# Kernel optimization log

Hardware: AMD Instinct MI355X
Metric: run time of the kernel (lower is better)

Reference implementation:

```python
import jax, jax.numpy as jnp
import numpy as np
from jax import lax

# Static config (matches init_kwargs)
DIM = 256; DR = 4; GROUP = 2; NH = 4; KS = 3; NA = 1; NUM_CLASS = 80; MUL = 5.0
CR = DIM // DR            # reduced dim = 64
GC = CR // GROUP          # offset-group channels = 32
HC = CR // NH             # per-head dim = 16
SCALE = HC ** -0.5
B, H, W = 8, 64, 64


def setup_inputs() -> dict:
    key = jax.random.key(0)
    ks_ = jax.random.split(key, 8)
    x = jax.random.normal(ks_[0], (B, DIM, H, W), jnp.float32)
    # offset = absolute pixel coordinates of the base sampling grid
    offset = jax.random.uniform(ks_[1], (B, NA * 2 * KS * KS, H, W), jnp.float32) * (H - 1)
    return dict(
        x=x, offset=offset,
        ln1_g=jnp.ones((DIM,), jnp.float32), ln1_b=jnp.zeros((DIM,), jnp.float32),
        w_qkv=jax.random.normal(ks_[2], (3 * CR, DIM), jnp.float32) * 0.02,
        w_dw=jax.random.normal(ks_[3], (GC, 1, 3, 3), jnp.float32) * 0.1,
        ln2_g=jnp.ones((GC,), jnp.float32), ln2_b=jnp.zeros((GC,), jnp.float32),
        w_off=jax.random.normal(ks_[4], (NA * 2 * KS * KS, GC, 3, 3), jnp.float32) * 0.02,
        b_off=jnp.zeros((NA * 2 * KS * KS,), jnp.float32),
        rpb_table=jax.random.normal(ks_[5], (1, NH, 1, 1, KS * KS, HC), jnp.float32) * 0.02,
        w_proj=jax.random.normal(ks_[6], (DIM, CR), jnp.float32) * 0.02,
        b_proj=jnp.zeros((DIM,), jnp.float32),
        w_cls=jax.random.normal(ks_[7], (NUM_CLASS, DIM), jnp.float32) * 0.02,
        b_cls=jnp.zeros((NUM_CLASS,), jnp.float32),
    )


def _ln_chw(x, g, b, eps=1e-5):
    # LayerNorm over channel dim of NCHW tensor (LayerNormProxy)
    xt = jnp.moveaxis(x, 1, -1)
    m = xt.mean(-1, keepdims=True)
    v = ((xt - m) ** 2).mean(-1, keepdims=True)
    y = (xt - m) * lax.rsqrt(v + eps) * g + b
    return jnp.moveaxis(y, -1, 1)


def _conv(x, w, groups=1, pad=1):
    return lax.conv_general_dilated(x, w, (1, 1), [(pad, pad), (pad, pad)],
                                    feature_group_count=groups,
                                    dimension_numbers=('NCHW', 'OIHW', 'NCHW'))


def _grid_sample(img, grid):
    # img [N,C,H,W]; grid [N,Ho,Wo,2] with (x,y) in [-1,1]; bilinear, zeros pad, align_corners=True
    N, C, Hi, Wi = img.shape
    gx = (grid[..., 0] + 1.0) * 0.5 * (Wi - 1)
    gy = (grid[..., 1] + 1.0) * 0.5 * (Hi - 1)
    x0 = jnp.floor(gx); y0 = jnp.floor(gy)
    x1 = x0 + 1.0;      y1 = y0 + 1.0

    def gather(ix, iy):
        valid = (ix >= 0) & (ix <= Wi - 1) & (iy >= 0) & (iy <= Hi - 1)
        ixc = jnp.clip(ix, 0, Wi - 1).astype(jnp.int32)
        iyc = jnp.clip(iy, 0, Hi - 1).astype(jnp.int32)
        v = jax.vmap(lambda im, yy, xx: im[:, yy, xx])(img, iyc, ixc)  # [N,C,Ho,Wo]
        return v * valid[:, None].astype(img.dtype)

    wa = ((x1 - gx) * (y1 - gy))[:, None]
    wb = ((gx - x0) * (y1 - gy))[:, None]
    wc = ((x1 - gx) * (gy - y0))[:, None]
    wd = ((gx - x0) * (gy - y0))[:, None]
    return (gather(x0, y0) * wa + gather(x1, y0) * wb +
            gather(x0, y1) * wc + gather(x1, y1) * wd)


def _extract_feats(feat, off, Hh, Ww):
    # feat [Bg,GC,H,W]; off [Bg, NA*2*KS*KS, H, W] in pixel coords (row, col)
    Bg = feat.shape[0]
    o = off.reshape(Bg, NA, KS, KS, 2, Hh, Ww)
    o = o.transpose(0, 1, 2, 5, 3, 6, 4)                  # b na kh h kw w d
    o = o.reshape(Bg, NA * KS * Hh, KS * Ww, 2)
    gy = 2.0 * o[..., 0] / (Hh - 1) - 1.0                  # row coord
    gx = 2.0 * o[..., 1] / (Ww - 1) - 1.0                  # col coord
    grid = jnp.stack([gx, gy], -1)                         # flip(-1): (x, y)
    out = _grid_sample(feat, grid)                         # [Bg,GC,NA*KS*H,KS*W]
    out = out.reshape(Bg, GC, NA, KS, Hh, KS, Ww)
    out = out.transpose(0, 2, 3, 5, 1, 4, 6).reshape(Bg, NA * KS * KS, GC, Hh, Ww)
    return out


def reference(x, offset, ln1_g, ln1_b, w_qkv, w_dw, ln2_g, ln2_b, w_off, b_off,
              rpb_table, w_proj, b_proj, w_cls, b_cls):
    Bb, C, Hh, Ww = x.shape
    N = KS * KS

    x_ = _ln_chw(x, ln1_g, ln1_b)
    qkv = jnp.einsum('oc,bchw->bohw', w_qkv, x_)           # [B,3*CR,H,W]
    q, k, v = jnp.split(qkv, 3, axis=1)                    # each [B,CR,H,W]

    # --- offset prediction ---
    q_off = q.reshape(Bb * GROUP, GC, Hh, Ww)
    t = _conv(q_off, w_dw, groups=GC)                      # depthwise 3x3
    t = _ln_chw(t, ln2_g, ln2_b)
    t = jax.nn.gelu(t, approximate=False)
    pred_offset = _conv(t, w_off) + b_off[None, :, None, None]

    off = jnp.broadcast_to(offset[:, None], (Bb, GROUP, NA * 2 * N, Hh, Ww))
    off = off.reshape(Bb * GROUP, NA * 2 * N, Hh, Ww)
    off = jnp.tanh(pred_offset) * MUL + off

    # --- deformable gather of k/v ---
    k = _extract_feats(k.reshape(Bb * GROUP, GC, Hh, Ww), off, Hh, Ww)
    v = _extract_feats(v.reshape(Bb * GROUP, GC, Hh, Ww), off, Hh, Ww)

    def to_heads(t):
        # [(b g), na*n, gc, h, w] -> [b, nh, hw, na, n, hc]
        t = t.reshape(Bb, GROUP, NA, N, GC, Hh, Ww)
        t = t.transpose(0, 5, 6, 2, 3, 1, 4)               # b h w na n g gc
        t = t.reshape(Bb, Hh * Ww, NA, N, NH, HC)
        return t.transpose(0, 4, 1, 2, 3, 5)

    k = to_heads(k) + rpb_table                            # [B,NH,HW,NA,N,HC]
    v = to_heads(v)

    q = q.reshape(Bb, NH, HC, Hh * Ww).transpose(0, 1, 3, 2)  # [B,NH,HW,HC]
    q = jnp.broadcast_to((q * SCALE)[:, :, :, None, :], (Bb, NH, Hh * Ww, NA, HC))

    attn = jnp.einsum('bnpac,bnpakc->bnpak', q, k)         # [B,NH,HW,NA,N]
    attn = jax.nn.softmax(attn, axis=-1)
    out = jnp.einsum('bnpak,bnpakc->bnpac', attn, v)       # [B,NH,HW,NA,HC]

    out = out.transpose(0, 2, 3, 1, 4).reshape(Bb, Hh * Ww, NA, CR)
    out = out @ w_proj.T + b_proj                          # [B,HW,NA,C]
    out = out + x.transpose(0, 2, 3, 1).reshape(Bb, Hh * Ww, 1, C)

    cls = out @ w_cls.T + b_cls                            # [B,HW,NA,NUM_CLASS]
    cls = cls.reshape(Bb, Hh, Ww, NA, NUM_CLASS).transpose(0, 3, 4, 1, 2)
    return cls.reshape(Bb, NA * NUM_CLASS, Hh, Ww)
```

## Files before the change

kernel.cpp:

```cpp
#include <hip/hip_runtime.h>
#include <hip/hip_fp16.h>
#include <math.h>

#define BB   8
#define HW   4096
#define BHW  32768
#define DIM  256
#define CR   64
#define GC   32
#define NHD  4
#define HC   16
#define NTAP 9
#define NCLS 80

#define OFF_QP   0u
#define OFF_QT   2097152u
#define OFF_KT   4194304u
#define OFF_T    8388608u
#define OFF_WBF  8388608u
#define OFF_AB   8437760u
#define OFF_OFFB 10485760u
#define OFF_AOT  11665408u
#define OFF_WPT  13762560u
#define OFF_WCT  13778944u
#define OFF_WFT  13799424u

typedef short bf16x8 __attribute__((ext_vector_type(8)));
typedef float f32x4  __attribute__((ext_vector_type(4)));

__device__ __forceinline__ unsigned short f2bf(float f) {
    unsigned u = __float_as_uint(f);
    unsigned r = u + 0x7FFFu + ((u >> 16) & 1u);
    return (unsigned short)(r >> 16);
}

__global__ __launch_bounds__(256) void k0_prep(
    const float* __restrict__ wqkv, const float* __restrict__ g1,
    const float* __restrict__ b1, const float* __restrict__ woff,
    const float* __restrict__ wproj, const float* __restrict__ wcls,
    float* __restrict__ ws)
{
    const int t = threadIdx.x;
    const int blk = blockIdx.x;
    if (blk < 192) {
        const int o = blk;
        unsigned short* wbf = (unsigned short*)(ws + OFF_WBF);
        wbf[o * 256 + t] = f2bf(wqkv[o * 256 + t] * g1[t]);
    } else if (blk < 448) {
        const int r = blk - 192;
        unsigned short* wpb = (unsigned short*)(ws + OFF_WPT);
        unsigned short* wcb = (unsigned short*)(ws + OFF_WCT);
        if (t < 64) wpb[r * 64 + t] = f2bf(wproj[r * 64 + t]);
        if (r < 80) wcb[r * 256 + t] = f2bf(wcls[r * 256 + t]);
    } else if (blk < 640) {
        const int o = blk - 448;
        __shared__ float sa[4], sb[4];
        float w = wqkv[o * 256 + t];
        float a = w * g1[t];
        float bb = w * b1[t];
        #pragma unroll
        for (int off = 1; off < 64; off <<= 1) {
            a  += __shfl_xor(a,  off, 64);
            bb += __shfl_xor(bb, off, 64);
        }
        const int wv = t >> 6;
        if ((t & 63) == 0) { sa[wv] = a; sb[wv] = bb; }
        __syncthreads();
        if (t == 0) {
            ws[OFF_AB + o]       = sa[0] + sa[1] + sa[2] + sa[3];
            ws[OFF_AB + 192 + o] = sb[0] + sb[1] + sb[2] + sb[3];
        }
    } else {
        int idx = (blk - 640) * 256 + t;
        if (idx < 5184) {
            int o = idx % 18;
            int rest = idx / 18;
            int ic = rest & 31, wo = rest >> 5;
            ws[OFF_WFT + idx] = woff[(o * 32 + ic) * 9 + wo];
        }
    }
}

__global__ __launch_bounds__(512) void k1_mfma(
    const float* __restrict__ x, float* __restrict__ ws)
{
    __shared__ float tile[64 * 193];
    const int t = threadIdx.x;
    const int b = blockIdx.x & 7, row = blockIdx.x >> 3;
    const int wv = __builtin_amdgcn_readfirstlane(t >> 6);
    const int pt = wv & 3, oh = wv >> 2;
    const int lane = t & 63;
    const int quad = lane >> 4, pxl = lane & 15;
    const int colbase = row * 64 + pt * 16 + pxl;
    const unsigned short* wbf = (const unsigned short*)(ws + OFF_WBF);
    const float* AB = ws + OFF_AB;

    f32x4 acc[6];
    #pragma unroll
    for (int ot = 0; ot < 6; ++ot) acc[ot] = (f32x4){0.f, 0.f, 0.f, 0.f};
    float s = 0.f, ss = 0.f;
    const size_t xb0 = (size_t)b * DIM * HW + colbase;

    for (int ks = 0; ks < 8; ++ks) {
        const int cbase = ks * 32 + quad * 8;
        float xv[8];
        #pragma unroll
        for (int j = 0; j < 8; ++j) {
            xv[j] = x[xb0 + (size_t)(cbase + j) * HW];
            s += xv[j]; ss += xv[j] * xv[j];
        }
        union { bf16x8 v; unsigned short u[8]; } bfrag;
        #pragma unroll
        for (int j = 0; j < 8; ++j) bfrag.u[j] = f2bf(xv[j]);
        #pragma unroll
        for (int ot = 0; ot < 6; ++ot) {
            const int orow = (oh * 6 + ot) * 16 + pxl;
            union { float4 f; bf16x8 v; } afrag;
            afrag.f = *(const float4*)&wbf[orow * 256 + cbase];
            acc[ot] = __builtin_amdgcn_mfma_f32_16x16x32_bf16(afrag.v, bfrag.v, acc[ot], 0, 0, 0);
        }
    }

    s  += __shfl_xor(s, 16, 64);  s  += __shfl_xor(s, 32, 64);
    ss += __shfl_xor(ss, 16, 64); ss += __shfl_xor(ss, 32, 64);
    const float m = s * (1.f / 256.f);
    const float rsv = rsqrtf(ss * (1.f / 256.f) - m * m + 1e-5f);

    const int px = pt * 16 + pxl;
    #pragma unroll
    for (int ot = 0; ot < 6; ++ot) {
        #pragma unroll
        for (int r = 0; r < 4; ++r) {
            int o = (oh * 6 + ot) * 16 + quad * 4 + r;
            tile[px * 193 + o] = rsv * (acc[ot][r] - m * AB[o]) + AB[192 + o];
        }
    }
    __syncthreads();

    float*  qp  = ws + OFF_QP;
    __half* qth = (__half*)(ws + OFF_QT);
    __half* kvh = (__half*)(ws + OFF_KT);
    const int colrow = row * 64;
    #pragma unroll
    for (int it = 0; it < 8; ++it) {
        int idx = it * 512 + t;
        int o = idx >> 6, px2 = idx & 63;
        qp[(size_t)(b * 64 + o) * HW + colrow + px2] = tile[px2 * 193 + o];
    }
    #pragma unroll
    for (int it = 0; it < 8; ++it) {
        int idx = it * 512 + t;
        int px2 = idx >> 6, o = idx & 63;
        qth[(size_t)(b * HW + colrow + px2) * 64 + o] = __float2half(tile[px2 * 193 + o]);
    }
    #pragma unroll
    for (int it = 0; it < 4; ++it) {
        int idx = it * 512 + t;
        int px2 = idx >> 5, ch32 = idx & 31;
        int sB = ch32 >> 4, ch = ch32 & 15;
        kvh[(size_t)((2 * b) * HW + colrow + px2) * 64 + sB * 32 + ch]
            = __float2half(tile[px2 * 193 + 64 + ch32]);
    }
    #pragma unroll
    for (int it = 0; it < 4; ++it) {
        int idx = it * 512 + t;
        int px2 = idx >> 5, ch32 = idx & 31;
        int sB = ch32 >> 4, ch = ch32 & 15;
        kvh[(size_t)((2 * b + 1) * HW + colrow + px2) * 64 + sB * 32 + ch]
            = __float2half(tile[px2 * 193 + 96 + ch32]);
    }
    #pragma unroll
    for (int it = 0; it < 4; ++it) {
        int idx = it * 512 + t;
        int px2 = idx >> 5, ch32 = idx & 31;
        int sB = ch32 >> 4, ch = ch32 & 15;
        kvh[(size_t)((2 * b) * HW + colrow + px2) * 64 + sB * 32 + 16 + ch]
            = __float2half(tile[px2 * 193 + 128 + ch32]);
    }
    #pragma unroll
    for (int it = 0; it < 4; ++it) {
        int idx = it * 512 + t;
        int px2 = idx >> 5, ch32 = idx & 31;
        int sB = ch32 >> 4, ch = ch32 & 15;
        kvh[(size_t)((2 * b + 1) * HW + colrow + px2) * 64 + sB * 32 + 16 + ch]
            = __float2half(tile[px2 * 193 + 160 + ch32]);
    }
}

__global__ __launch_bounds__(256) void k2_off_feat(
    const float* __restrict__ wdw, const float* __restrict__ g2, const float* __restrict__ b2,
    float* __restrict__ ws)
{
    __shared__ float qtile[3][32][64];
    __shared__ float rsum[4][64], rsq[4][64], smv[64], srv[64];
    const int t = threadIdx.x;
    const int b = blockIdx.x & 7;
    const int rest = blockIdx.x >> 3;
    const int g = rest & 1;
    const int row = rest >> 1;
    const int bg = b * 2 + g;
    const int p = t & 63;
    const int cq = __builtin_amdgcn_readfirstlane(t >> 6);
    const float* qp = ws + OFF_QP;

    #pragma unroll
    for (int it = 0; it < 6; ++it) {
        int idx = it * 256 + t;
        int rc = idx >> 4;
        int seg = (idx & 15) << 2;
        int dyy = rc >> 5, ch = rc & 31;
        int y = row + dyy - 1;
        float4 v = make_float4(0.f, 0.f, 0.f, 0.f);
        if ((unsigned)y < 64u)
            v = *(const float4*)&qp[(size_t)(b * 64 + g * 32 + ch) * HW + y * 64 + seg];
        *(float4*)&qtile[dyy][ch][seg] = v;
    }
    __syncthreads();

    float vals[8];
    float s = 0.f, ss = 0.f;
    #pragma unroll
    for (int i = 0; i < 8; ++i) {
        int ch = cq * 8 + i;
        float a = 0.f;
        #pragma unroll
        for (int dy = 0; dy < 3; ++dy) {
            #pragma unroll
            for (int dx = 0; dx < 3; ++dx) {
                int xx = p + dx - 1;
                bool vld = (unsigned)xx < 64u;
                float q = qtile[dy][ch][vld ? xx : 0];
                a += (vld ? q : 0.f) * wdw[ch * 9 + dy * 3 + dx];
            }
        }
        vals[i] = a; s += a; ss += a * a;
    }
    rsum[cq][p] = s; rsq[cq][p] = ss;
    __syncthreads();
    if (t < 64) {
        float S = rsum[0][t] + rsum[1][t] + rsum[2][t] + rsum[3][t];
        float Q = rsq[0][t] + rsq[1][t] + rsq[2][t] + rsq[3][t];
        float m = S * (1.f / 32.f);
        float v = Q * (1.f / 32.f) - m * m;
        smv[t] = m; srv[t] = rsqrtf(v + 1e-5f);
    }
    __syncthreads();
    float m = smv[p], rv = srv[p];
    float* tb = ws + OFF_T;
    #pragma unroll
    for (int i = 0; i < 8; ++i) {
        int ch = cq * 8 + i;
        float u = (vals[i] - m) * rv * g2[ch] + b2[ch];
        float ge = 0.5f * u * (1.f + erff(u * 0.70710678118654752f));
        tb[(size_t)(bg * 32 + ch) * HW + row * 64 + p] = ge;
    }
}

__global__ __launch_bounds__(256) void k3_pred_off(
    const float* __restrict__ boff, const float* __restrict__ off_in,
    float* __restrict__ ws)
{
    __shared__ float part[4 * 18 * 64];
    const int t = threadIdx.x;
    const int b = blockIdx.x & 7;
    const int rest = blockIdx.x >> 3;
    const int g = rest & 1;
    const int row = rest >> 1;
    const int bg = b * 2 + g;
    const int p = t & 63;
    const int icq = __builtin_amdgcn_readfirstlane(t >> 6);
    const float* tb = ws + OFF_T;
    const float* wfT = ws + OFF_WFT;
    float acc[18];
    #pragma unroll
    for (int o = 0; o < 18; ++o) acc[o] = 0.f;
    #pragma unroll
    for (int dy = 0; dy < 3; ++dy) {
        int y = row + dy - 1;
        if ((unsigned)y >= 64u) continue;
        #pragma unroll
        for (int dx = 0; dx < 3; ++dx) {
            int xx = p + dx - 1;
            bool vld = (unsigned)xx < 64u;
            int xc = vld ? xx : 0;
            int wo = dy * 3 + dx;
            #pragma unroll
            for (int i = 0; i < 8; ++i) {
                int ic = icq * 8 + i;
                float tv = tb[(size_t)(bg * 32 + ic) * HW + y * 64 + xc];
                tv = vld ? tv : 0.f;
                const float* wrow = wfT + (wo * 32 + ic) * 18;
                #pragma unroll
                for (int o = 0; o < 18; ++o)
                    acc[o] += tv * wrow[o];
            }
        }
    }
    #pragma unroll
    for (int o = 0; o < 18; ++o) part[(icq * 18 + o) * 64 + p] = acc[o];
    __syncthreads();
    float* ob = ws + OFF_OFFB;
    #pragma unroll
    for (int r = 0; r < 5; ++r) {
        int idx = t + r * 256;
        if (idx < 1152) {
            int o = idx >> 6, p2 = idx & 63;
            float v = part[o * 64 + p2] + part[(18 + o) * 64 + p2]
                    + part[(36 + o) * 64 + p2] + part[(54 + o) * 64 + p2] + boff[o];
            v = tanhf(v) * 5.0f + off_in[(size_t)(b * 18 + o) * HW + row * 64 + p2];
            ob[(size_t)(bg * 18 + o) * HW + row * 64 + p2] = v;
        }
    }
}

__global__ __launch_bounds__(256, 4) void k4_attn(
    const float* __restrict__ rpb, float* __restrict__ ws)
{
    __shared__ float rpb_l[NHD * NTAP * HC];
    for (int i = threadIdx.x; i < NHD * NTAP * HC; i += 256) rpb_l[i] = rpb[i];
    __syncthreads();

    const int t = threadIdx.x;
    const int wave = __builtin_amdgcn_readfirstlane(t >> 6);
    const int g = wave & 1, pxh = wave >> 1;
    const int lane = t & 63;
    const int pxl = lane & 7;
    const int prt = lane >> 3;
    const int s    = prt >> 2;
    const int half = (prt >> 1) & 1;
    const int j    = prt & 1;
    const int b = blockIdx.x & 7;
    const int chunk = blockIdx.x >> 3;
    const int hw = chunk * 16 + pxh * 8 + pxl;
    const int pix = b * HW + hw;
    const int bg = b * 2 + g;
    const int head = g * 2 + s;

    const __half* qth = (const __half*)(ws + OFF_QT);
    const __half* kvh = (const __half*)(ws + OFF_KT);
    const float*  ob  = ws + OFF_OFFB;

    float rr_[NTAP], cc_[NTAP];
    #pragma unroll
    for (int n = 0; n < NTAP; ++n) {
        rr_[n] = ob[(size_t)(bg * 18 + 2 * n) * HW + hw];
        cc_[n] = ob[(size_t)(bg * 18 + 2 * n + 1) * HW + hw];
    }

    union F4H { float4 f; __half2 h[4]; };
    F4H qld;
    qld.f = *(const float4*)&qth[(size_t)pix * 64 + g * 32 + s * 16 + j * 8];
    const float qs = half ? 0.0f : 0.25f;
    float qv[8];
    #pragma unroll
    for (int i = 0; i < 4; ++i) {
        float2 q2 = __half22float2(qld.h[i]);
        qv[2 * i] = q2.x * qs; qv[2 * i + 1] = q2.y * qs;
    }

    const float4* rb4 = (const float4*)(rpb_l + head * (NTAP * HC) + j * 8);
    const __half* kvp = kvh + (size_t)(bg * HW) * 64 + prt * 8;

    __half2 av[NTAP][4];
    float logit[NTAP];

    #pragma unroll
    for (int n = 0; n < NTAP; ++n) {
        float r = rr_[n];
        float c = cc_[n];
        float y0f = floorf(r), x0f = floorf(c);
        float fy = r - y0f, fx = c - x0f;
        int iy0 = (int)y0f, ix0 = (int)x0f;
        float wts[4] = { (1.f - fx) * (1.f - fy), fx * (1.f - fy),
                         (1.f - fx) * fy,         fx * fy };
        __half2 acc0 = __float2half2_rn(0.f), acc1 = acc0, acc2 = acc0, acc3 = acc0;
        #pragma unroll
        for (int corner = 0; corner < 4; ++corner) {
            int cxx = ix0 + (corner & 1);
            int cyy = iy0 + (corner >> 1);
            bool vld = ((unsigned)cxx < 64u) && ((unsigned)cyy < 64u);
            float w = vld ? wts[corner] : 0.f;
            int cxc = min(max(cxx, 0), 63);
            int cyc = min(max(cyy, 0), 63);
            F4H kv;
            kv.f = *(const float4*)&kvp[(size_t)(cyc * 64 + cxc) * 64];
            __half2 w2 = __float2half2_rn(w);
            acc0 = __hfma2(kv.h[0], w2, acc0);
            acc1 = __hfma2(kv.h[1], w2, acc1);
            acc2 = __hfma2(kv.h[2], w2, acc2);
            acc3 = __hfma2(kv.h[3], w2, acc3);
        }
        av[n][0] = acc0; av[n][1] = acc1; av[n][2] = acc2; av[n][3] = acc3;
        float4 r0 = rb4[n * 4], r1 = rb4[n * 4 + 1];
        float2 a0 = __half22float2(acc0), a1 = __half22float2(acc1);
        float2 a2 = __half22float2(acc2), a3 = __half22float2(acc3);
        float part = qv[0] * (a0.x + r0.x) + qv[1] * (a0.y + r0.y)
                   + qv[2] * (a1.x + r0.z) + qv[3] * (a1.y + r0.w)
                   + qv[4] * (a2.x + r1.x) + qv[5] * (a2.y + r1.y)
                   + qv[6] * (a3.x + r1.z) + qv[7] * (a3.y + r1.w);
        part += __shfl_xor(part, 8, 64);
        part += __shfl_xor(part, 16, 64);
        logit[n] = part;
    }

    float m = logit[0];
    #pragma unroll
    for (int n = 1; n < NTAP; ++n) m = fmaxf(m, logit[n]);
    float l = 0.f;
    #pragma unroll
    for (int n = 0; n < NTAP; ++n) { logit[n] = __expf(logit[n] - m); l += logit[n]; }
    const float inv = 1.f / l;

    __half2 o0 = __float2half2_rn(0.f), o1 = o0, o2 = o0, o3 = o0;
    #pragma unroll
    for (int n = 0; n < NTAP; ++n) {
        __half2 p2 = __float2half2_rn(logit[n]);
        o0 = __hfma2(av[n][0], p2, o0);
        o1 = __hfma2(av[n][1], p2, o1);
        o2 = __hfma2(av[n][2], p2, o2);
        o3 = __hfma2(av[n][3], p2, o3);
    }
    if (half) {
        unsigned short* aob = (unsigned short*)(ws + OFF_AOT);
        const int cb = head * 16 + j * 8;
        float2 f0 = __half22float2(o0), f1 = __half22float2(o1);
        float2 f2 = __half22float2(o2), f3 = __half22float2(o3);
        union { float4 f; unsigned short u[8]; } pk;
        pk.u[0] = f2bf(f0.x * inv); pk.u[1] = f2bf(f0.y * inv);
        pk.u[2] = f2bf(f1.x * inv); pk.u[3] = f2bf(f1.y * inv);
        pk.u[4] = f2bf(f2.x * inv); pk.u[5] = f2bf(f2.y * inv);
        pk.u[6] = f2bf(f3.x * inv); pk.u[7] = f2bf(f3.y * inv);
        *(float4*)&aob[(size_t)pix * 64 + cb] = pk.f;
    }
}

__global__ __launch_bounds__(256) void k5_mfma(
    const float* __restrict__ x, const float* __restrict__ bproj,
    const float* __restrict__ bcls, float* __restrict__ ws, float* __restrict__ out)
{
    __shared__ unsigned short tmp[64][264];
    const int t = threadIdx.x;
    const int b = blockIdx.x & 7, row = blockIdx.x >> 3;
    const int wv = __builtin_amdgcn_readfirstlane(t >> 6);
    const int lane = t & 63, quad = lane >> 4, pxl = lane & 15;
    const int px = wv * 16 + pxl;
    const int pixcol = row * 64 + px;
    const size_t pix = (size_t)b * HW + pixcol;
    const unsigned short* aob = (const unsigned short*)(ws + OFF_AOT);
    const unsigned short* wpb = (const unsigned short*)(ws + OFF_WPT);
    const unsigned short* wcb = (const unsigned short*)(ws + OFF_WCT);

    union FB { float4 f; bf16x8 v; };
    FB bf0, bf1;
    bf0.f = *(const float4*)&aob[pix * 64 + quad * 8];
    bf1.f = *(const float4*)&aob[pix * 64 + 32 + quad * 8];

    #pragma unroll 4
    for (int ot = 0; ot < 16; ++ot) {
        f32x4 acc = (f32x4){0.f, 0.f, 0.f, 0.f};
        FB a0, a1;
        const int om = ot * 16 + pxl;
        a0.f = *(const float4*)&wpb[om * 64 + quad * 8];
        a1.f = *(const float4*)&wpb[om * 64 + 32 + quad * 8];
        acc = __builtin_amdgcn_mfma_f32_16x16x32_bf16(a0.v, bf0.v, acc, 0, 0, 0);
        acc = __builtin_amdgcn_mfma_f32_16x16x32_bf16(a1.v, bf1.v, acc, 0, 0, 0);
        union { unsigned short u[4]; ushort2 s2[2]; } pk;
        #pragma unroll
        for (int r = 0; r < 4; ++r) {
            int o = ot * 16 + quad * 4 + r;
            float v = acc[r] + bproj[o] + x[(size_t)(b * DIM + o) * HW + pixcol];
            pk.u[r] = f2bf(v);
        }
        *(ushort4*)&tmp[px][ot * 16 + quad * 4] = *(ushort4*)pk.u;
    }
    __syncthreads();

    f32x4 acc2[5];
    #pragma unroll
    for (int oc = 0; oc < 5; ++oc) acc2[oc] = (f32x4){0.f, 0.f, 0.f, 0.f};
    #pragma unroll
    for (int kc = 0; kc < 8; ++kc) {
        FB bb;
        bb.f = *(const float4*)&tmp[px][kc * 32 + quad * 8];
        #pragma unroll
        for (int oc = 0; oc < 5; ++oc) {
            FB aa;
            aa.f = *(const float4*)&wcb[(oc * 16 + pxl) * 256 + kc * 32 + quad * 8];
            acc2[oc] = __builtin_amdgcn_mfma_f32_16x16x32_bf16(aa.v, bb.v, acc2[oc], 0, 0, 0);
        }
    }
    #pragma unroll
    for (int oc = 0; oc < 5; ++oc) {
        #pragma unroll
        for (int r = 0; r < 4; ++r) {
            int o = oc * 16 + quad * 4 + r;
            out[(size_t)(b * NCLS + o) * HW + pixcol] = acc2[oc][r] + bcls[o];
        }
    }
}

extern "C" void kernel_launch(void* const* d_in, const int* in_sizes, int n_in,
                              void* d_out, int out_size, void* d_ws, size_t ws_size,
                              hipStream_t stream)
{
    const float* x     = (const float*)d_in[0];
    const float* off   = (const float*)d_in[1];
    const float* g1    = (const float*)d_in[2];
    const float* b1    = (const float*)d_in[3];
    const float* wqkv  = (const float*)d_in[4];
    const float* wdw   = (const float*)d_in[5];
    const float* g2    = (const float*)d_in[6];
    const float* b2    = (const float*)d_in[7];
    const float* woff  = (const float*)d_in[8];
    const float* boff  = (const float*)d_in[9];
    const float* rpb   = (const float*)d_in[10];
    const float* wproj = (const float*)d_in[11];
    const float* bproj = (const float*)d_in[12];
    const float* wcls  = (const float*)d_in[13];
    const float* bcls  = (const float*)d_in[14];
    float* ws  = (float*)d_ws;
    float* out = (float*)d_out;

    hipLaunchKernelGGL(k0_prep,     dim3(661),  dim3(256), 0, stream, wqkv, g1, b1, woff, wproj, wcls, ws);
    hipLaunchKernelGGL(k1_mfma,     dim3(512),  dim3(512), 0, stream, x, ws);
    hipLaunchKernelGGL(k2_off_feat, dim3(1024), dim3(256), 0, stream, wdw, g2, b2, ws);
    hipLaunchKernelGGL(k3_pred_off, dim3(1024), dim3(256), 0, stream, boff, off, ws);
    hipLaunchKernelGGL(k4_attn,     dim3(2048), dim3(256), 0, stream, rpb, ws);
    hipLaunchKernelGGL(k5_mfma,     dim3(512),  dim3(256), 0, stream, x, bproj, bcls, ws, out);
}
```

Baseline: 231.3 us.

## Compute offset-prediction conv with fp16 MFMA over channel-last fp16 features

The 3x3 offset-prediction convolution (32 in, 18 out channels) now runs as fp16 MFMA 16x16x32 products instead of scalar FMA loops. To feed it, the offset-feature kernel writes its GELU output as channel-last fp16 (8 channels packed per 16-byte store), and the prep kernel packs the offset weights into an fp16 MFMA A-operand layout padded to 32 outputs. This removes the scalar inner loop and the shared-memory partial-sum reduction, and halves the intermediate tensor's traffic. The cost is fp16 rounding of activations and weights, plus wasted MFMA work on the padded output rows.

Result: faster. 218.7 us (-5.5%).

```diff
diff --git a/kernel.cpp b/kernel.cpp
--- a/kernel.cpp
+++ b/kernel.cpp
@@ -16,17 +16,18 @@
 #define OFF_QP   0u
 #define OFF_QT   2097152u
 #define OFF_KT   4194304u
-#define OFF_T    8388608u
 #define OFF_WBF  8388608u
 #define OFF_AB   8437760u
+#define OFF_T16  8650752u
 #define OFF_OFFB 10485760u
 #define OFF_AOT  11665408u
 #define OFF_WPT  13762560u
 #define OFF_WCT  13778944u
 #define OFF_WFT  13799424u
 
-typedef short bf16x8 __attribute__((ext_vector_type(8)));
-typedef float f32x4  __attribute__((ext_vector_type(4)));
+typedef short    bf16x8 __attribute__((ext_vector_type(8)));
+typedef _Float16 f16x8  __attribute__((ext_vector_type(8)));
+typedef float    f32x4  __attribute__((ext_vector_type(4)));
 
 __device__ __forceinline__ unsigned short f2bf(float f) {
     unsigned u = __float_as_uint(f);
@@ -72,11 +73,15 @@
         }
     } else {
         int idx = (blk - 640) * 256 + t;
-        if (idx < 5184) {
-            int o = idx % 18;
-            int rest = idx / 18;
-            int ic = rest & 31, wo = rest >> 5;
-            ws[OFF_WFT + idx] = woff[(o * 32 + ic) * 9 + wo];
+        if (idx < 2 * 9 * 64 * 8) {
+            int j = idx & 7;
+            int lane = (idx >> 3) & 63;
+            int mw = idx >> 9;
+            int m = mw / 9, wo = mw % 9;
+            int o = m * 16 + (lane & 15);
+            int ic = (lane >> 4) * 8 + j;
+            float v = (o < 18) ? woff[(o * 32 + ic) * 9 + wo] : 0.f;
+            ((__half*)(ws + OFF_WFT))[idx] = __float2half(v);
         }
     }
 }
@@ -246,69 +251,79 @@
     }
     __syncthreads();
     float m = smv[p], rv = srv[p];
-    float* tb = ws + OFF_T;
+    __half* tb16 = (__half*)(ws + OFF_T16);
     #pragma unroll
     for (int i = 0; i < 8; ++i) {
         int ch = cq * 8 + i;
         float u = (vals[i] - m) * rv * g2[ch] + b2[ch];
-        float ge = 0.5f * u * (1.f + erff(u * 0.70710678118654752f));
-        tb[(size_t)(bg * 32 + ch) * HW + row * 64 + p] = ge;
-    }
-}
-
-__global__ __launch_bounds__(256) void k3_pred_off(
+        vals[i] = 0.5f * u * (1.f + erff(u * 0.70710678118654752f));
+    }
+    union { float4 f; __half2 h[4]; } o16;
+    #pragma unroll
+    for (int i = 0; i < 4; ++i) o16.h[i] = __floats2half2_rn(vals[2 * i], vals[2 * i + 1]);
+    *(float4*)&tb16[((size_t)bg * HW + row * 64 + p) * 32 + cq * 8] = o16.f;
+}
+
+__global__ __launch_bounds__(256) void k3_mfma(
     const float* __restrict__ boff, const float* __restrict__ off_in,
     float* __restrict__ ws)
 {
-    __shared__ float part[4 * 18 * 64];
     const int t = threadIdx.x;
     const int b = blockIdx.x & 7;
     const int rest = blockIdx.x >> 3;
     const int g = rest & 1;
-    const int row = rest >> 1;
+    const int rowgrp = (rest >> 1) & 15;
+    const int xh = rest >> 5;
+    const int wv = __builtin_amdgcn_readfirstlane(t >> 6);
+    const int lane = t & 63;
+    const int quad = lane >> 4, pxl = lane & 15;
+    const int row = rowgrp * 4 + wv;
     const int bg = b * 2 + g;
-    const int p = t & 63;
-    const int icq = __builtin_amdgcn_readfirstlane(t >> 6);
-    const float* tb = ws + OFF_T;
-    const float* wfT = ws + OFF_WFT;
-    float acc[18];
-    #pragma unroll
-    for (int o = 0; o < 18; ++o) acc[o] = 0.f;
-    #pragma unroll
-    for (int dy = 0; dy < 3; ++dy) {
-        int y = row + dy - 1;
-        if ((unsigned)y >= 64u) continue;
-        #pragma unroll
-        for (int dx = 0; dx < 3; ++dx) {
-            int xx = p + dx - 1;
-            bool vld = (unsigned)xx < 64u;
-            int xc = vld ? xx : 0;
-            int wo = dy * 3 + dx;
+    const __half* t16 = (const __half*)(ws + OFF_T16);
+    const __half* wfA = (const __half*)(ws + OFF_WFT);
+
+    f32x4 acc[2][2];
+    #pragma unroll
+    for (int i = 0; i < 2; ++i)
+        #pragma unroll
+        for (int j = 0; j < 2; ++j) acc[i][j] = (f32x4){0.f, 0.f, 0.f, 0.f};
+
+    union FH { float4 f; f16x8 h; };
+    #pragma unroll
+    for (int wo = 0; wo < 9; ++wo) {
+        const int dy = wo / 3, dx = wo % 3;
+        const int y = row + dy - 1;
+        const bool yv = (unsigned)y < 64u;
+        FH a0, a1;
+        a0.f = *(const float4*)&wfA[(size_t)((0 * 9 + wo) * 64 + lane) * 8];
+        a1.f = *(const float4*)&wfA[(size_t)((1 * 9 + wo) * 64 + lane) * 8];
+        #pragma unroll
+        for (int tile = 0; tile < 2; ++tile) {
+            const int x = xh * 32 + tile * 16 + pxl + dx - 1;
+            FH bf;
+            bf.f = make_float4(0.f, 0.f, 0.f, 0.f);
+            if (yv && (unsigned)x < 64u)
+                bf.f = *(const float4*)&t16[((size_t)bg * HW + y * 64 + x) * 32 + quad * 8];
+            acc[tile][0] = __builtin_amdgcn_mfma_f32_16x16x32_f16(a0.h, bf.h, acc[tile][0], 0, 0, 0);
+            acc[tile][1] = __builtin_amdgcn_mfma_f32_16x16x32_f16(a1.h, bf.h, acc[tile][1], 0, 0, 0);
+        }
+    }
+
+    float* ob = ws + OFF_OFFB;
+    #pragma unroll
+    for (int tile = 0; tile < 2; ++tile) {
+        const int px = xh * 32 + tile * 16 + pxl;
+        #pragma unroll
+        for (int mi = 0; mi < 2; ++mi) {
             #pragma unroll
-            for (int i = 0; i < 8; ++i) {
-                int ic = icq * 8 + i;
-                float tv = tb[(size_t)(bg * 32 + ic) * HW + y * 64 + xc];
-                tv = vld ? tv : 0.f;
-                const float* wrow = wfT + (wo * 32 + ic) * 18;
-                #pragma unroll
-                for (int o = 0; o < 18; ++o)
-                    acc[o] += tv * wrow[o];
+            for (int r = 0; r < 4; ++r) {
+                int o = mi * 16 + quad * 4 + r;
+                if (o < 18) {
+                    float v = acc[tile][mi][r] + boff[o];
+                    v = tanhf(v) * 5.0f + off_in[(size_t)(b * 18 + o) * HW + row * 64 + px];
+                    ob[(size_t)(bg * 18 + o) * HW + row * 64 + px] = v;
+                }
             }
-        }
-    }
-    #pragma unroll
-    for (int o = 0; o < 18; ++o) part[(icq * 18 + o) * 64 + p] = acc[o];
-    __syncthreads();
-    float* ob = ws + OFF_OFFB;
-    #pragma unroll
-    for (int r = 0; r < 5; ++r) {
-        int idx = t + r * 256;
-        if (idx < 1152) {
-            int o = idx >> 6, p2 = idx & 63;
-            float v = part[o * 64 + p2] + part[(18 + o) * 64 + p2]
-                    + part[(36 + o) * 64 + p2] + part[(54 + o) * 64 + p2] + boff[o];
-            v = tanhf(v) * 5.0f + off_in[(size_t)(b * 18 + o) * HW + row * 64 + p2];
-            ob[(size_t)(bg * 18 + o) * HW + row * 64 + p2] = v;
         }
     }
 }
@@ -521,10 +536,10 @@
     float* ws  = (float*)d_ws;
     float* out = (float*)d_out;
 
-    hipLaunchKernelGGL(k0_prep,     dim3(661),  dim3(256), 0, stream, wqkv, g1, b1, woff, wproj, wcls, ws);
+    hipLaunchKernelGGL(k0_prep,     dim3(676),  dim3(256), 0, stream, wqkv, g1, b1, woff, wproj, wcls, ws);
     hipLaunchKernelGGL(k1_mfma,     dim3(512),  dim3(512), 0, stream, x, ws);
     hipLaunchKernelGGL(k2_off_feat, dim3(1024), dim3(256), 0, stream, wdw, g2, b2, ws);
-    hipLaunchKernelGGL(k3_pred_off, dim3(1024), dim3(256), 0, stream, boff, off, ws);
+    hipLaunchKernelGGL(k3_mfma,     dim3(512),  dim3(256), 0, stream, boff, off, ws);
     hipLaunchKernelGGL(k4_attn,     dim3(2048), dim3(256), 0, stream, rpb, ws);
     hipLaunchKernelGGL(k5_mfma,     dim3(512),  dim3(256), 0, stream, x, bproj, bcls, ws, out);
 }
```
